# Performance work log

Hardware: AMD Instinct MI355X
Metric: run time of the kernel (lower is better)

Reference implementation:

```python
import jax, jax.numpy as jnp
import numpy as np


def setup_inputs() -> dict:
    key = jax.random.key(0)
    k1, k2, k3 = jax.random.split(key, 3)
    B, Lc, Lq, D = 16, 1024, 1024, 256
    context_features = jax.random.normal(k1, (B, Lc, D), dtype=jnp.float32)
    question_features = jax.random.normal(k2, (B, Lq, D), dtype=jnp.float32)
    # nn.Linear(3D, 1, bias=False) weight, stored transposed as [3D, 1]
    weight = jax.random.normal(k3, (3 * D, 1), dtype=jnp.float32) * (1.0 / np.sqrt(3 * D))
    return {"context_features": context_features, "question_features": question_features, "weight": weight}


def reference(context_features, question_features, weight):
    # Trilinear similarity: sim[b,i,j] = [c_i ; q_j ; c_i*q_j] @ w
    # Decompose w = [wc ; wq ; wm] (each D) to avoid the O(B*Lc*Lq*3D) tensor:
    # sim = c@wc + q@wq + (c*wm) @ q^T   -- exact same math as the concat+Linear.
    D = context_features.shape[-1]
    w = weight[:, 0]
    wc, wq, wm = w[:D], w[D:2 * D], w[2 * D:]
    sim = (
        jnp.einsum('bcd,d->bc', context_features, wc)[:, :, None]
        + jnp.einsum('bqd,d->bq', question_features, wq)[:, None, :]
        + jnp.einsum('bcd,bqd->bcq', context_features * wm, question_features)
    )  # [B, Lc, Lq]
    weight_c2q = jax.nn.softmax(sim, axis=-1)                      # [B, Lc, Lq]
    c2q = jnp.einsum('bcq,bqd->bcd', weight_c2q, question_features)
    weight_q2c = jax.nn.softmax(jnp.max(sim, axis=2), axis=-1)     # [B, Lc]
    q2c = jnp.einsum('bc,bcd->bd', weight_q2c, context_features)   # [B, D]
    q2c = jnp.broadcast_to(q2c[:, None, :], c2q.shape)             # repeat over Lc
    return (c2q, q2c)
```

## Files before the change

kernel.cpp:

```cpp
#include <hip/hip_runtime.h>
#include <math.h>

#define BB 16
#define LC 1024
#define LQ 1024
#define DD 256

#define CTB 64
#define QTB 64
#define QT_S 72

typedef __attribute__((ext_vector_type(4))) float f32x4;
typedef __attribute__((ext_vector_type(8))) short bf16x8;
typedef __attribute__((ext_vector_type(4))) short bf16x4;

__device__ inline short f2bf(float f) {
    union { float f; unsigned u; } v; v.f = f;
    unsigned r = v.u + 0x7FFFu + ((v.u >> 16) & 1u);
    return (short)(r >> 16);
}


__global__ __launch_bounds__(256) void k_terms(const float* __restrict__ ctx,
                                               const float* __restrict__ qst,
                                               const float* __restrict__ w,
                                               float* __restrict__ ws) {
    int gw = (blockIdx.x * 256 + threadIdx.x) >> 6;
    int lane = threadIdx.x & 63;
    bool isQ = gw >= BB * LC;
    int row = isQ ? gw - BB * LC : gw;
    const float* src = isQ ? qst : ctx;
    const float* wp  = isQ ? (w + DD) : w;
    float4 x  = *(const float4*)(src + (size_t)row * DD + lane * 4);
    float4 wv = *(const float4*)(wp + lane * 4);
    float d = x.x * wv.x + x.y * wv.y + x.z * wv.z + x.w * wv.w;
    #pragma unroll
    for (int off = 32; off; off >>= 1) d += __shfl_xor(d, off);
    float* dst = ws + (isQ ? 0 : BB * LQ);
    if (lane == 0) dst[row] = d;
}

__global__ __launch_bounds__(256) void k_prep(const float* __restrict__ qst,
                                              short* __restrict__ Qbf,
                                              short* __restrict__ Qtbf) {
    __shared__ short Qt_lds[DD][QT_S];
    int t = threadIdx.x;
    int qt = blockIdx.x;
    int b  = blockIdx.y;
    int wv4 = t >> 6;
    int l   = t & 63;
    int lx  = l & 15;
    int ls  = l >> 4;

    #pragma unroll
    for (int kq = 0; kq < 4; ++kq) {
        #pragma unroll
        for (int jd = 0; jd < 4; ++jd) {
            int ql = 16 * wv4 + 4 * kq + ls;
            int d0 = 64 * jd + 4 * lx;
            float4 x = *(const float4*)(qst + ((size_t)(b * LQ + qt * QTB + ql)) * DD + d0);
            bf16x4 o;
            o[0] = f2bf(x.x); o[1] = f2bf(x.y); o[2] = f2bf(x.z); o[3] = f2bf(x.w);
            *(bf16x4*)(Qbf + ((size_t)(b * LQ + qt * QTB + ql)) * DD + d0) = o;
            float X[4] = {x.x, x.y, x.z, x.w};
            float P1[4], X1[4], P2[4], X2[4];
            #pragma unroll
            for (int e = 0; e < 4; ++e) P1[e] = __shfl_xor(X[e ^ 1], 16);
            #pragma unroll
            for (int e = 0; e < 4; ++e) X1[e] = ((ls & 1) == (e & 1)) ? X[e] : P1[e];
            #pragma unroll
            for (int e = 0; e < 4; ++e) P2[e] = __shfl_xor(X1[e ^ 2], 32);
            #pragma unroll
            for (int e = 0; e < 4; ++e) X2[e] = ((ls & 2) == (e & 2)) ? X1[e] : P2[e];
            int dl = 64 * jd + 4 * lx + ls;
            bf16x4 ot;
            ot[0] = f2bf(X2[0]); ot[1] = f2bf(X2[1]); ot[2] = f2bf(X2[2]); ot[3] = f2bf(X2[3]);
            *(bf16x4*)&Qt_lds[dl][16 * wv4 + 4 * kq] = ot;
        }
    }
    __syncthreads();
    #pragma unroll
    for (int rep = 0; rep < 8; ++rep) {
        int d   = rep * 32 + (t >> 3);
        int qch = t & 7;
        bf16x8 v = *(const bf16x8*)&Qt_lds[d][8 * qch];
        *(bf16x8*)(Qtbf + ((size_t)(b * DD + d)) * LQ + qt * QTB + 8 * qch) = v;
    }
}

__global__ __launch_bounds__(512) void k_main(const float* __restrict__ ctx,
                                              const short* __restrict__ Qbf,
                                              const short* __restrict__ Qtbf,
                                              const float* __restrict__ wght,
                                              const float* __restrict__ ws,
                                              float* __restrict__ out,
                                              float* __restrict__ rowmax_out) {
    __shared__ short CMp[4 * 8 * 512];
    __shared__ short sPp[2][4 * 2 * 512];
    __shared__ float scaleS[2][CTB];
    __shared__ float mS[2][CTB], lS[2][CTB];
    __shared__ float mergebuf[4 * 64 * 20];

    const int t  = threadIdx.x;
    const int wv = t >> 6;
    const int g  = wv >> 2;
    const int w4 = wv & 3;
    const int l  = t & 63;
    const int lx = l & 15;
    const int ls = l >> 4;
    const int b  = blockIdx.y;
    const int c0 = blockIdx.x * CTB;

    const float* qterm = ws;
    const float* cterm = ws + BB * LQ;

    {
        const int kh = g * 4;
        int cl = 16 * w4 + lx;
        #pragma unroll
        for (int kq = 0; kq < 4; ++kq) {
            int kk = kh + kq;
            int d0 = 32 * kk + 8 * ls;
            const float4 x0 = *(const float4*)(ctx + ((size_t)(b * LC + c0 + cl)) * DD + d0);
            const float4 x1 = *(const float4*)(ctx + ((size_t)(b * LC + c0 + cl)) * DD + d0 + 4);
            const float4 w0 = *(const float4*)(wght + 2 * DD + d0);
            const float4 w1 = *(const float4*)(wght + 2 * DD + d0 + 4);
            bf16x8 o;
            o[0] = f2bf(x0.x * w0.x); o[1] = f2bf(x0.y * w0.y);
            o[2] = f2bf(x0.z * w0.z); o[3] = f2bf(x0.w * w0.w);
            o[4] = f2bf(x1.x * w1.x); o[5] = f2bf(x1.y * w1.y);
            o[6] = f2bf(x1.z * w1.z); o[7] = f2bf(x1.w * w1.w);
            *(bf16x8*)&CMp[(w4 * 8 + kk) * 512 + l * 8] = o;
        }
    }

    float mrun[4], lrun[4];
    f32x4 oacc[4][4];
    #pragma unroll
    for (int r = 0; r < 4; ++r) { mrun[r] = -1e30f; lrun[r] = 0.f; }
    #pragma unroll
    for (int cf = 0; cf < 4; ++cf)
        #pragma unroll
        for (int df = 0; df < 4; ++df)
            oacc[cf][df] = (f32x4){0.f, 0.f, 0.f, 0.f};

    __syncthreads();

    for (int it = 0; it < 8; ++it) {
        const int qtile = 2 * it + g;
        const size_t qbase = (size_t)b * LQ + qtile * QTB;

        float qv[4];
        #pragma unroll
        for (int f = 0; f < 4; ++f) qv[f] = qterm[qbase + 16 * f + lx];

        f32x4 sacc[4];
        #pragma unroll
        for (int f = 0; f < 4; ++f) sacc[f] = (f32x4){0.f, 0.f, 0.f, 0.f};
        bf16x8 aP[2], bP[2][4];
        aP[0] = *(const bf16x8*)&CMp[(w4 * 8 + 0) * 512 + l * 8];
        #pragma unroll
        for (int f = 0; f < 4; ++f)
            bP[0][f] = *(const bf16x8*)(Qbf + (qbase + 16 * f + lx) * DD + 8 * ls);
        #pragma unroll
        for (int kk = 0; kk < 8; ++kk) {
            int cur = kk & 1, nxt = cur ^ 1;
            if (kk < 7) {
                aP[nxt] = *(const bf16x8*)&CMp[(w4 * 8 + kk + 1) * 512 + l * 8];
                #pragma unroll
                for (int f = 0; f < 4; ++f)
                    bP[nxt][f] = *(const bf16x8*)(Qbf + (qbase + 16 * f + lx) * DD + 32 * (kk + 1) + 8 * ls);
            }
            #pragma unroll
            for (int f = 0; f < 4; ++f)
                sacc[f] = __builtin_amdgcn_mfma_f32_16x16x32_bf16(aP[cur], bP[cur][f], sacc[f], 0, 0, 0);
        }

        #pragma unroll
        for (int f = 0; f < 4; ++f) {
            #pragma unroll
            for (int r = 0; r < 4; ++r) sacc[f][r] += qv[f];
        }
        float scl[4];
        #pragma unroll
        for (int r = 0; r < 4; ++r) {
            float v = fmaxf(fmaxf(sacc[0][r], sacc[1][r]), fmaxf(sacc[2][r], sacc[3][r]));
            v = fmaxf(v, __shfl_xor(v, 1));
            v = fmaxf(v, __shfl_xor(v, 2));
            v = fmaxf(v, __shfl_xor(v, 4));
            v = fmaxf(v, __shfl_xor(v, 8));
            float mn = fmaxf(mrun[r], v);
            scl[r] = __expf(mrun[r] - mn);
            mrun[r] = mn;
            lrun[r] *= scl[r];
        }
        float p[4][4];
        float rs[4] = {0.f, 0.f, 0.f, 0.f};
        #pragma unroll
        for (int f = 0; f < 4; ++f)
            #pragma unroll
            for (int r = 0; r < 4; ++r) {
                p[f][r] = __expf(sacc[f][r] - mrun[r]);
                rs[r] += p[f][r];
            }
        #pragma unroll
        for (int r = 0; r < 4; ++r) {
            float v = rs[r];
            v += __shfl_xor(v, 1);
            v += __shfl_xor(v, 2);
            v += __shfl_xor(v, 4);
            v += __shfl_xor(v, 8);
            lrun[r] += v;
        }
        #pragma unroll
        for (int f = 0; f < 4; ++f) {
            #pragma unroll
            for (int r = 0; r < 4; ++r) {
                int cl = 16 * w4 + 4 * ls + r;
                int ql = 16 * f + lx;
                int idx = ((cl >> 4) * 2 + (ql >> 5)) * 512 + ((cl & 15) + 16 * ((ql >> 3) & 3)) * 8 + (ql & 7);
                sPp[g][idx] = f2bf(p[f][r]);
            }
        }
        if (lx == 0) {
            #pragma unroll
            for (int r = 0; r < 4; ++r) scaleS[g][16 * w4 + 4 * ls + r] = scl[r];
        }
        __syncthreads();

        #pragma unroll
        for (int cf = 0; cf < 4; ++cf) {
            #pragma unroll
            for (int r = 0; r < 4; ++r) {
                float s = scaleS[g][16 * cf + 4 * ls + r];
                #pragma unroll
                for (int df = 0; df < 4; ++df) oacc[cf][df][r] *= s;
            }
        }
        #pragma unroll
        for (int kk = 0; kk < 2; ++kk) {
            bf16x8 pa[4], qb[4];
            #pragma unroll
            for (int cf = 0; cf < 4; ++cf)
                pa[cf] = *(const bf16x8*)&sPp[g][(cf * 2 + kk) * 512 + l * 8];
            #pragma unroll
            for (int df = 0; df < 4; ++df)
                qb[df] = *(const bf16x8*)(Qtbf + ((size_t)(b * DD + 64 * w4 + 16 * df + lx)) * LQ
                                          + qtile * QTB + 32 * kk + 8 * ls);
            #pragma unroll
            for (int df = 0; df < 4; ++df)
                #pragma unroll
                for (int cf = 0; cf < 4; ++cf)
                    oacc[cf][df] = __builtin_amdgcn_mfma_f32_16x16x32_bf16(pa[cf], qb[df], oacc[cf][df], 0, 0, 0);
        }
        __syncthreads();
    }

    if (lx == 0) {
        #pragma unroll
        for (int r = 0; r < 4; ++r) {
            mS[g][16 * w4 + 4 * ls + r] = mrun[r];
            lS[g][16 * w4 + 4 * ls + r] = lrun[r];
        }
    }
    __syncthreads();

    float alpha[4][4], ltot[4][4], mtot[4][4];
    #pragma unroll
    for (int cf = 0; cf < 4; ++cf) {
        #pragma unroll
        for (int r = 0; r < 4; ++r) {
            int cl = 16 * cf + 4 * ls + r;
            float m0 = mS[0][cl], m1 = mS[1][cl];
            float mx = fmaxf(m0, m1);
            float a0 = __expf(m0 - mx), a1 = __expf(m1 - mx);
            mtot[cf][r] = mx;
            ltot[cf][r] = a0 * lS[0][cl] + a1 * lS[1][cl];
            alpha[cf][r] = (g == 0) ? a0 : a1;
        }
    }
    #pragma unroll
    for (int cf = 0; cf < 4; ++cf) {
        #pragma unroll
        for (int df = 0; df < 4; ++df)
            #pragma unroll
            for (int r = 0; r < 4; ++r)
                oacc[cf][df][r] *= alpha[cf][r];
    }
    #pragma unroll
    for (int cf = 0; cf < 4; ++cf) {
        if (g == 1) {
            #pragma unroll
            for (int df = 0; df < 4; ++df)
                *(f32x4*)&mergebuf[(w4 * 64 + l) * 20 + df * 4] = oacc[cf][df];
        }
        __syncthreads();
        if (g == 0) {
            #pragma unroll
            for (int df = 0; df < 4; ++df) {
                f32x4 v = *(const f32x4*)&mergebuf[(w4 * 64 + l) * 20 + df * 4];
                oacc[cf][df][0] += v[0]; oacc[cf][df][1] += v[1];
                oacc[cf][df][2] += v[2]; oacc[cf][df][3] += v[3];
            }
        }
        __syncthreads();
    }

    if (g == 0) {
        if (wv == 0 && lx == 0) {
            #pragma unroll
            for (int cf = 0; cf < 4; ++cf)
                #pragma unroll
                for (int r = 0; r < 4; ++r) {
                    int c = b * LC + c0 + 16 * cf + 4 * ls + r;
                    rowmax_out[c] = mtot[cf][r] + cterm[c];
                }
        }
        #pragma unroll
        for (int cf = 0; cf < 4; ++cf) {
            #pragma unroll
            for (int r = 0; r < 4; ++r) {
                float inv = 1.0f / ltot[cf][r];
                size_t row = (size_t)(b * LC + c0 + 16 * cf + 4 * ls + r) * DD;
                #pragma unroll
                for (int df = 0; df < 4; ++df)
                    out[row + 64 * w4 + 16 * df + lx] = oacc[cf][df][r] * inv;
            }
        }
    }
}

__global__ __launch_bounds__(256) void k_q2c(const float* __restrict__ ctx,
                                             const float* __restrict__ rowmax,
                                             float* __restrict__ q2cvec) {
    __shared__ float sm[LC];
    __shared__ float red[256];
    int b = blockIdx.x;
    int chunk = blockIdx.y;
    int t = threadIdx.x;
    const float* rm = rowmax + b * LC;

    float lmax = -1e30f;
    #pragma unroll
    for (int k = 0; k < 4; ++k) {
        float v = rm[t + k * 256];
        sm[t + k * 256] = v;
        lmax = fmaxf(lmax, v);
    }
    red[t] = lmax;
    __syncthreads();
    for (int s = 128; s > 0; s >>= 1) {
        if (t < s) red[t] = fmaxf(red[t], red[t + s]);
        __syncthreads();
    }
    float gmax = red[0];
    __syncthreads();
    float lsum = 0.f;
    #pragma unroll
    for (int k = 0; k < 4; ++k) {
        int i = t + k * 256;
        float e = __expf(sm[i] - gmax);
        sm[i] = e;
        lsum += e;
    }
    red[t] = lsum;
    __syncthreads();
    for (int s = 128; s > 0; s >>= 1) {
        if (t < s) red[t] += red[t + s];
        __syncthreads();
    }
    float inv = 1.0f / red[0];

    int c0 = chunk * 32;
    float acc = 0.f;
    for (int c = c0; c < c0 + 32; ++c)
        acc += sm[c] * ctx[(size_t)(b * LC + c) * DD + t];
    atomicAdd(&q2cvec[b * DD + t], acc * inv);
}

__global__ __launch_bounds__(256) void k_bcast(const float* __restrict__ q2cvec,
                                               float* __restrict__ out2) {
    int g = blockIdx.x * 256 + threadIdx.x;
    int b  = g >> 16;
    int d4 = g & 63;
    ((float4*)out2)[g] = ((const float4*)q2cvec)[b * 64 + d4];
}

extern "C" void kernel_launch(void* const* d_in, const int* in_sizes, int n_in,
                              void* d_out, int out_size, void* d_ws, size_t ws_size,
                              hipStream_t stream) {
    const float* ctx = (const float*)d_in[0];
    const float* qst = (const float*)d_in[1];
    const float* w   = (const float*)d_in[2];
    float* out  = (float*)d_out;
    float* out2 = out + (size_t)BB * LC * DD;
    float* ws   = (float*)d_ws;

    float* rowmax = ws + 32768;
    float* q2cvec = ws + 49152;
    short* Qbf  = (short*)out2;
    short* Qtbf = Qbf + (size_t)BB * LQ * DD;

    hipMemsetAsync(q2cvec, 0, BB * DD * sizeof(float), stream);

    k_terms<<<(2 * BB * LC) / 4, 256, 0, stream>>>(ctx, qst, w, ws);

    k_prep<<<dim3(LQ / QTB, BB), 256, 0, stream>>>(qst, Qbf, Qtbf);

    k_main<<<dim3(LC / CTB, BB), 512, 0, stream>>>(ctx, Qbf, Qtbf, w, ws, out, rowmax);

    k_q2c<<<dim3(BB, 32), 256, 0, stream>>>(ctx, rowmax, q2cvec);

    k_bcast<<<(BB * LC * DD / 4) / 256, 256, 0, stream>>>(q2cvec, out2);
}
```

Measured before the change: 197.8 us.

## Fuse term dot-products into prep/main kernels and restructure Q-load prefetch

Removes the separate k_terms kernel. The q-term dot products are now computed inside k_prep while the question rows are being read, and the c-term dot products inside k_main while it stages ctx into shared memory. This saves one launch and a second full read of ctx and qst. The block index mapping in k_main is also changed so consecutive blocks walk across batches, and the Q operand loads are issued in larger batches, with the Qt loads hoisted ahead of the softmax, to overlap global latency with MFMA work. The larger batched loads raise register pressure.

Measured after the change: 185.9 us. -6.0%, faster.

```diff
diff --git a/kernel.cpp b/kernel.cpp
--- a/kernel.cpp
+++ b/kernel.cpp
@@ -21,28 +21,11 @@
 }
 
 
-__global__ __launch_bounds__(256) void k_terms(const float* __restrict__ ctx,
-                                               const float* __restrict__ qst,
-                                               const float* __restrict__ w,
-                                               float* __restrict__ ws) {
-    int gw = (blockIdx.x * 256 + threadIdx.x) >> 6;
-    int lane = threadIdx.x & 63;
-    bool isQ = gw >= BB * LC;
-    int row = isQ ? gw - BB * LC : gw;
-    const float* src = isQ ? qst : ctx;
-    const float* wp  = isQ ? (w + DD) : w;
-    float4 x  = *(const float4*)(src + (size_t)row * DD + lane * 4);
-    float4 wv = *(const float4*)(wp + lane * 4);
-    float d = x.x * wv.x + x.y * wv.y + x.z * wv.z + x.w * wv.w;
-    #pragma unroll
-    for (int off = 32; off; off >>= 1) d += __shfl_xor(d, off);
-    float* dst = ws + (isQ ? 0 : BB * LQ);
-    if (lane == 0) dst[row] = d;
-}
-
 __global__ __launch_bounds__(256) void k_prep(const float* __restrict__ qst,
+                                              const float* __restrict__ w,
                                               short* __restrict__ Qbf,
-                                              short* __restrict__ Qtbf) {
+                                              short* __restrict__ Qtbf,
+                                              float* __restrict__ qterm) {
     __shared__ short Qt_lds[DD][QT_S];
     int t = threadIdx.x;
     int qt = blockIdx.x;
@@ -54,11 +37,14 @@
 
     #pragma unroll
     for (int kq = 0; kq < 4; ++kq) {
+        int ql = 16 * wv4 + 4 * kq + ls;
+        float qpart = 0.f;
         #pragma unroll
         for (int jd = 0; jd < 4; ++jd) {
-            int ql = 16 * wv4 + 4 * kq + ls;
             int d0 = 64 * jd + 4 * lx;
             float4 x = *(const float4*)(qst + ((size_t)(b * LQ + qt * QTB + ql)) * DD + d0);
+            float4 wq = *(const float4*)(w + DD + d0);
+            qpart += x.x * wq.x + x.y * wq.y + x.z * wq.z + x.w * wq.w;
             bf16x4 o;
             o[0] = f2bf(x.x); o[1] = f2bf(x.y); o[2] = f2bf(x.z); o[3] = f2bf(x.w);
             *(bf16x4*)(Qbf + ((size_t)(b * LQ + qt * QTB + ql)) * DD + d0) = o;
@@ -77,6 +63,11 @@
             ot[0] = f2bf(X2[0]); ot[1] = f2bf(X2[1]); ot[2] = f2bf(X2[2]); ot[3] = f2bf(X2[3]);
             *(bf16x4*)&Qt_lds[dl][16 * wv4 + 4 * kq] = ot;
         }
+        qpart += __shfl_xor(qpart, 1);
+        qpart += __shfl_xor(qpart, 2);
+        qpart += __shfl_xor(qpart, 4);
+        qpart += __shfl_xor(qpart, 8);
+        if (lx == 0) qterm[b * LQ + qt * QTB + ql] = qpart;
     }
     __syncthreads();
     #pragma unroll
@@ -99,6 +90,7 @@
     __shared__ short sPp[2][4 * 2 * 512];
     __shared__ float scaleS[2][CTB];
     __shared__ float mS[2][CTB], lS[2][CTB];
+    __shared__ float ctermS[2][CTB];
     __shared__ float mergebuf[4 * 64 * 20];
 
     const int t  = threadIdx.x;
@@ -108,15 +100,16 @@
     const int l  = t & 63;
     const int lx = l & 15;
     const int ls = l >> 4;
-    const int b  = blockIdx.y;
-    const int c0 = blockIdx.x * CTB;
+    const int bid = blockIdx.x;
+    const int b  = bid & 15;
+    const int c0 = (bid >> 4) * CTB;
 
     const float* qterm = ws;
-    const float* cterm = ws + BB * LQ;
 
     {
         const int kh = g * 4;
         int cl = 16 * w4 + lx;
+        float cpart = 0.f;
         #pragma unroll
         for (int kq = 0; kq < 4; ++kq) {
             int kk = kh + kq;
@@ -125,6 +118,10 @@
             const float4 x1 = *(const float4*)(ctx + ((size_t)(b * LC + c0 + cl)) * DD + d0 + 4);
             const float4 w0 = *(const float4*)(wght + 2 * DD + d0);
             const float4 w1 = *(const float4*)(wght + 2 * DD + d0 + 4);
+            const float4 c0v = *(const float4*)(wght + d0);
+            const float4 c1v = *(const float4*)(wght + d0 + 4);
+            cpart += x0.x * c0v.x + x0.y * c0v.y + x0.z * c0v.z + x0.w * c0v.w
+                   + x1.x * c1v.x + x1.y * c1v.y + x1.z * c1v.z + x1.w * c1v.w;
             bf16x8 o;
             o[0] = f2bf(x0.x * w0.x); o[1] = f2bf(x0.y * w0.y);
             o[2] = f2bf(x0.z * w0.z); o[3] = f2bf(x0.w * w0.w);
@@ -132,6 +129,9 @@
             o[6] = f2bf(x1.z * w1.z); o[7] = f2bf(x1.w * w1.w);
             *(bf16x8*)&CMp[(w4 * 8 + kk) * 512 + l * 8] = o;
         }
+        cpart += __shfl_xor(cpart, 16);
+        cpart += __shfl_xor(cpart, 32);
+        if (ls == 0) ctermS[g][cl] = cpart;
     }
 
     float mrun[4], lrun[4];
@@ -150,32 +150,47 @@
         const int qtile = 2 * it + g;
         const size_t qbase = (size_t)b * LQ + qtile * QTB;
 
+        f32x4 sacc[4];
+        #pragma unroll
+        for (int f = 0; f < 4; ++f) sacc[f] = (f32x4){0.f, 0.f, 0.f, 0.f};
+        bf16x8 bA[4][4], bB[4][4];
+        #pragma unroll
+        for (int kk = 0; kk < 4; ++kk)
+            #pragma unroll
+            for (int f = 0; f < 4; ++f)
+                bA[kk][f] = *(const bf16x8*)(Qbf + (qbase + 16 * f + lx) * DD + 32 * kk + 8 * ls);
+        bf16x8 acur = *(const bf16x8*)&CMp[(w4 * 8 + 0) * 512 + l * 8];
+        #pragma unroll
+        for (int kk = 0; kk < 4; ++kk) {
+            bf16x8 anext = *(const bf16x8*)&CMp[(w4 * 8 + kk + 1) * 512 + l * 8];
+            #pragma unroll
+            for (int f = 0; f < 4; ++f)
+                bB[kk][f] = *(const bf16x8*)(Qbf + (qbase + 16 * f + lx) * DD + 32 * (kk + 4) + 8 * ls);
+            #pragma unroll
+            for (int f = 0; f < 4; ++f)
+                sacc[f] = __builtin_amdgcn_mfma_f32_16x16x32_bf16(acur, bA[kk][f], sacc[f], 0, 0, 0);
+            acur = anext;
+        }
+        #pragma unroll
+        for (int kk = 4; kk < 8; ++kk) {
+            bf16x8 anext = (kk < 7) ? *(const bf16x8*)&CMp[(w4 * 8 + kk + 1) * 512 + l * 8] : acur;
+            #pragma unroll
+            for (int f = 0; f < 4; ++f)
+                sacc[f] = __builtin_amdgcn_mfma_f32_16x16x32_bf16(acur, bB[kk - 4][f], sacc[f], 0, 0, 0);
+            acur = anext;
+        }
+
+        bf16x8 qtb[2][4];
+        #pragma unroll
+        for (int kk = 0; kk < 2; ++kk)
+            #pragma unroll
+            for (int df = 0; df < 4; ++df)
+                qtb[kk][df] = *(const bf16x8*)(Qtbf + ((size_t)(b * DD + 64 * w4 + 16 * df + lx)) * LQ
+                                               + qtile * QTB + 32 * kk + 8 * ls);
+
         float qv[4];
         #pragma unroll
         for (int f = 0; f < 4; ++f) qv[f] = qterm[qbase + 16 * f + lx];
-
-        f32x4 sacc[4];
-        #pragma unroll
-        for (int f = 0; f < 4; ++f) sacc[f] = (f32x4){0.f, 0.f, 0.f, 0.f};
-        bf16x8 aP[2], bP[2][4];
-        aP[0] = *(const bf16x8*)&CMp[(w4 * 8 + 0) * 512 + l * 8];
-        #pragma unroll
-        for (int f = 0; f < 4; ++f)
-            bP[0][f] = *(const bf16x8*)(Qbf + (qbase + 16 * f + lx) * DD + 8 * ls);
-        #pragma unroll
-        for (int kk = 0; kk < 8; ++kk) {
-            int cur = kk & 1, nxt = cur ^ 1;
-            if (kk < 7) {
-                aP[nxt] = *(const bf16x8*)&CMp[(w4 * 8 + kk + 1) * 512 + l * 8];
-                #pragma unroll
-                for (int f = 0; f < 4; ++f)
-                    bP[nxt][f] = *(const bf16x8*)(Qbf + (qbase + 16 * f + lx) * DD + 32 * (kk + 1) + 8 * ls);
-            }
-            #pragma unroll
-            for (int f = 0; f < 4; ++f)
-                sacc[f] = __builtin_amdgcn_mfma_f32_16x16x32_bf16(aP[cur], bP[cur][f], sacc[f], 0, 0, 0);
-        }
-
         #pragma unroll
         for (int f = 0; f < 4; ++f) {
             #pragma unroll
@@ -237,22 +252,19 @@
                 for (int df = 0; df < 4; ++df) oacc[cf][df][r] *= s;
             }
         }
-        #pragma unroll
-        for (int kk = 0; kk < 2; ++kk) {
-            bf16x8 pa[4], qb[4];
+        bf16x8 pa[2][4];
+        #pragma unroll
+        for (int kk = 0; kk < 2; ++kk)
             #pragma unroll
             for (int cf = 0; cf < 4; ++cf)
-                pa[cf] = *(const bf16x8*)&sPp[g][(cf * 2 + kk) * 512 + l * 8];
-            #pragma unroll
-            for (int df = 0; df < 4; ++df)
-                qb[df] = *(const bf16x8*)(Qtbf + ((size_t)(b * DD + 64 * w4 + 16 * df + lx)) * LQ
-                                          + qtile * QTB + 32 * kk + 8 * ls);
+                pa[kk][cf] = *(const bf16x8*)&sPp[g][(cf * 2 + kk) * 512 + l * 8];
+        #pragma unroll
+        for (int kk = 0; kk < 2; ++kk)
             #pragma unroll
             for (int df = 0; df < 4; ++df)
                 #pragma unroll
                 for (int cf = 0; cf < 4; ++cf)
-                    oacc[cf][df] = __builtin_amdgcn_mfma_f32_16x16x32_bf16(pa[cf], qb[df], oacc[cf][df], 0, 0, 0);
-        }
+                    oacc[cf][df] = __builtin_amdgcn_mfma_f32_16x16x32_bf16(pa[kk][cf], qtb[kk][df], oacc[cf][df], 0, 0, 0);
         __syncthreads();
     }
 
@@ -312,8 +324,9 @@
             for (int cf = 0; cf < 4; ++cf)
                 #pragma unroll
                 for (int r = 0; r < 4; ++r) {
-                    int c = b * LC + c0 + 16 * cf + 4 * ls + r;
-                    rowmax_out[c] = mtot[cf][r] + cterm[c];
+                    int cl = 16 * cf + 4 * ls + r;
+                    int c = b * LC + c0 + cl;
+                    rowmax_out[c] = mtot[cf][r] + ctermS[0][cl] + ctermS[1][cl];
                 }
         }
         #pragma unroll
@@ -396,6 +409,7 @@
     float* out2 = out + (size_t)BB * LC * DD;
     float* ws   = (float*)d_ws;
 
+    float* qterm  = ws;
     float* rowmax = ws + 32768;
     float* q2cvec = ws + 49152;
     short* Qbf  = (short*)out2;
@@ -403,11 +417,9 @@
 
     hipMemsetAsync(q2cvec, 0, BB * DD * sizeof(float), stream);
 
-    k_terms<<<(2 * BB * LC) / 4, 256, 0, stream>>>(ctx, qst, w, ws);
-
-    k_prep<<<dim3(LQ / QTB, BB), 256, 0, stream>>>(qst, Qbf, Qtbf);
-
-    k_main<<<dim3(LC / CTB, BB), 512, 0, stream>>>(ctx, Qbf, Qtbf, w, ws, out, rowmax);
+    k_prep<<<dim3(LQ / QTB, BB), 256, 0, stream>>>(qst, w, Qbf, Qtbf, qterm);
+
+    k_main<<<(LC / CTB) * BB, 512, 0, stream>>>(ctx, Qbf, Qtbf, w, ws, out, rowmax);
 
     k_q2c<<<dim3(BB, 32), 256, 0, stream>>>(ctx, rowmax, q2cvec);
 
```
